# Kernel optimization log

Hardware: AMD Instinct MI355X
Metric: run time of the kernel (lower is better)

The kernel has to match this reference:

```python
import jax, jax.numpy as jnp
import numpy as np

TOP_K = 32
SCALE_FACTOR = 8.0
NEG_INF = -1e18


def setup_inputs() -> dict:
    key = jax.random.key(0)
    kq, kk, kv = jax.random.split(key, 3)
    B, H, S, D = 2, 16, 2048, 64
    q = jax.random.normal(kq, (B, H, S, D), dtype=jnp.float32)
    k = jax.random.normal(kk, (B, H, S, D), dtype=jnp.float32)
    v = jax.random.normal(kv, (B, H, S, D), dtype=jnp.float32)
    return {"q": q, "k": k, "v": v}


def reference(q, k, v):
    # scores: [B, H, Sq, Sk]
    scores = jnp.einsum("bhqd,bhkd->bhqk", q, k) / SCALE_FACTOR
    # torch code clamps top_k against key.size()[-1] == head dim D (quirk);
    # with TOP_K=32 < D=64 the clamp is inactive.
    top_k = min(TOP_K, k.shape[-1])
    topv, _ = jax.lax.top_k(scores, top_k)            # [B,H,Sq,top_k], sorted desc
    thresh = topv[..., -1:]                            # k-th largest per query row
    mask_k = scores < thresh                           # True -> masked out
    scores = jnp.where(mask_k, NEG_INF, scores)
    attn = jax.nn.softmax(scores, axis=-1)
    context = jnp.einsum("bhqk,bhkd->bhqd", attn, v)
    return context, attn, mask_k
```

## Files before the change

kernel.cpp:

```cpp
#include <hip/hip_runtime.h>
#include <math.h>

namespace {
constexpr int kS = 2048;
constexpr int kD = 64;
constexpr int kBH = 32;
constexpr int kTopK = 32;
constexpr int kBins = 4096;
constexpr int kMaxCand = 256;
constexpr int kKeepCap = 64;
constexpr size_t kCtxElems  = (size_t)kBH * kS * kD;
constexpr size_t kAttnElems = (size_t)kBH * kS * kS;
}

__device__ __forceinline__ unsigned sortable_bits(float x) {
  unsigned u = __float_as_uint(x);
  return u ^ ((u & 0x80000000u) ? 0xFFFFFFFFu : 0x80000000u);
}

__global__ __launch_bounds__(256) void qk_scores(const float* __restrict__ q,
                                                 const float* __restrict__ k,
                                                 float* __restrict__ scores) {
  __shared__ float Qs[64][68];
  __shared__ float KsT[64][68];
  const int bh  = blockIdx.z;
  const int q0  = blockIdx.y * 64;
  const int k0  = blockIdx.x * 64;
  const int tid = threadIdx.x;
  const float* qg = q + ((size_t)bh * kS + q0) * kD;
  const float* kg = k + ((size_t)bh * kS + k0) * kD;

#pragma unroll
  for (int rnd = 0; rnd < 4; ++rnd) {
    int flat = rnd * 1024 + tid * 4;
    int r = flat >> 6;
    int c = flat & 63;
    float4 qv = *(const float4*)(qg + r * kD + c);
    *(float4*)(&Qs[r][c]) = qv;
    float4 kv = *(const float4*)(kg + r * kD + c);
    KsT[c + 0][r] = kv.x;
    KsT[c + 1][r] = kv.y;
    KsT[c + 2][r] = kv.z;
    KsT[c + 3][r] = kv.w;
  }
  __syncthreads();

  const int ty = tid >> 4;
  const int tx = tid & 15;
  float acc[4][4] = {};
#pragma unroll
  for (int kk = 0; kk < 64; kk += 4) {
    float4 a[4], b[4];
#pragma unroll
    for (int i = 0; i < 4; ++i) a[i] = *(const float4*)(&Qs[ty * 4 + i][kk]);
#pragma unroll
    for (int u = 0; u < 4; ++u) b[u] = *(const float4*)(&KsT[kk + u][tx * 4]);
    const float* Af = (const float*)a;
    const float* Bf = (const float*)b;
#pragma unroll
    for (int i = 0; i < 4; ++i)
#pragma unroll
      for (int u = 0; u < 4; ++u)
#pragma unroll
        for (int j = 0; j < 4; ++j)
          acc[i][j] += Af[i * 4 + u] * Bf[u * 4 + j];
  }

#pragma unroll
  for (int i = 0; i < 4; ++i) {
    float4 o = make_float4(acc[i][0] * 0.125f, acc[i][1] * 0.125f,
                           acc[i][2] * 0.125f, acc[i][3] * 0.125f);
    *(float4*)(scores + ((size_t)bh * kS + q0 + ty * 4 + i) * kS + k0 + tx * 4) = o;
  }
}

__global__ __launch_bounds__(256) void topk_softmax(const float* __restrict__ v,
                                                    float* __restrict__ ctx,
                                                    float* __restrict__ attn,
                                                    float* __restrict__ mask) {
  const int row  = blockIdx.x;
  const int bh   = row >> 11;
  const int tid  = threadIdx.x;
  const int lane = tid & 63;
  const int wid  = tid >> 6;

  __shared__ unsigned s_hist[kBins];
  __shared__ float    s_cand[kMaxCand];
  __shared__ int      s_kidx[kKeepCap];
  __shared__ float    s_kw[kKeepCap];
  __shared__ float    s_wmax[4], s_wsum[4];
  __shared__ unsigned s_T[4];
  __shared__ unsigned s_nc, s_nk;
  __shared__ int      s_bstar, s_gabove;
  __shared__ float    s_t32;

  const float* srow = attn + (size_t)row * kS;
  float4 l0 = *(const float4*)(srow + tid * 4);
  float4 l1 = *(const float4*)(srow + 1024 + tid * 4);
  float locv[8] = {l0.x, l0.y, l0.z, l0.w, l1.x, l1.y, l1.z, l1.w};
  int   loce[8];
#pragma unroll
  for (int j = 0; j < 8; ++j)
    loce[j] = (j < 4) ? (tid * 4 + j) : (1024 + tid * 4 + (j - 4));
#pragma unroll
  for (int i = 0; i < 4; ++i)
    *(uint4*)(&s_hist[tid * 16 + i * 4]) = make_uint4(0u, 0u, 0u, 0u);
  if (tid == 0) { s_nc = 0u; s_nk = 0u; }
  __syncthreads();

  unsigned bins[8];
  float pmax = locv[0];
#pragma unroll
  for (int j = 0; j < 8; ++j) {
    bins[j] = sortable_bits(locv[j]) >> 20;
    atomicAdd(&s_hist[bins[j]], 1u);
    pmax = fmaxf(pmax, locv[j]);
  }
#pragma unroll
  for (int off = 32; off >= 1; off >>= 1)
    pmax = fmaxf(pmax, __shfl_xor(pmax, off));
  if (lane == 0) s_wmax[wid] = pmax;
  __syncthreads();

  unsigned lsum = 0;
#pragma unroll
  for (int j = 0; j < 16; ++j) lsum += s_hist[tid * 16 + j];
  unsigned sfx = lsum;
#pragma unroll
  for (int off = 1; off < 64; off <<= 1) {
    unsigned z = __shfl_down(sfx, off);
    if (lane + off < 64) sfx += z;
  }
  if (lane == 0) s_T[wid] = sfx;
  __syncthreads();

  unsigned hi = 0;
#pragma unroll
  for (int w = 0; w < 4; ++w)
    if (w > wid) hi += s_T[w];
  unsigned gsfx  = sfx + hi;
  unsigned above = gsfx - lsum;
  if (gsfx >= (unsigned)kTopK && above < (unsigned)kTopK) {
    unsigned run = above;
    for (int j = 15; j >= 0; --j) {
      unsigned h = s_hist[tid * 16 + j];
      if (run < (unsigned)kTopK && run + h >= (unsigned)kTopK) {
        s_bstar  = tid * 16 + j;
        s_gabove = (int)run;
      }
      run += h;
    }
  }
  __syncthreads();
  const int   bstar  = s_bstar;
  const int   gabove = s_gabove;
  const float mx = fmaxf(fmaxf(s_wmax[0], s_wmax[1]),
                         fmaxf(s_wmax[2], s_wmax[3]));

#pragma unroll
  for (int j = 0; j < 8; ++j) {
    if ((int)bins[j] == bstar) {
      unsigned pos = atomicAdd(&s_nc, 1u);
      if (pos < (unsigned)kMaxCand) s_cand[pos] = locv[j];
    }
  }
  __syncthreads();
  const int m2 = (int)min(s_nc, (unsigned)kMaxCand);

  for (int c = tid; c < m2; c += 256) {
    float x = s_cand[c];
    int g = 0, e = 0;
    for (int j2 = 0; j2 < m2; ++j2) {
      float y = s_cand[j2];
      g += (y > x);
      e += (y == x);
    }
    int G = gabove + g;
    if (G < kTopK && G + e >= kTopK) s_t32 = x;
  }
  __syncthreads();
  const float t32 = s_t32;

  float w8[8];
  float psum = 0.0f;
#pragma unroll
  for (int j = 0; j < 8; ++j) {
    bool keep = (locv[j] >= t32);
    float wv = keep ? __expf(locv[j] - mx) : 0.0f;
    w8[j] = wv;
    psum += wv;
    if (keep) {
      unsigned p = atomicAdd(&s_nk, 1u);
      if (p < (unsigned)kKeepCap) { s_kidx[p] = loce[j]; s_kw[p] = wv; }
    }
  }
#pragma unroll
  for (int off = 32; off >= 1; off >>= 1)
    psum += __shfl_xor(psum, off);
  if (lane == 0) s_wsum[wid] = psum;
  __syncthreads();

  const float Z = s_wsum[0] + s_wsum[1] + s_wsum[2] + s_wsum[3];
  const float invZ = 1.0f / Z;

  float* arow = attn + (size_t)row * kS;
  float* mrow = mask + (size_t)row * kS;
  float4 a0 = make_float4(w8[0] * invZ, w8[1] * invZ, w8[2] * invZ, w8[3] * invZ);
  float4 a1 = make_float4(w8[4] * invZ, w8[5] * invZ, w8[6] * invZ, w8[7] * invZ);
  float4 m0 = make_float4(locv[0] >= t32 ? 0.f : 1.f, locv[1] >= t32 ? 0.f : 1.f,
                          locv[2] >= t32 ? 0.f : 1.f, locv[3] >= t32 ? 0.f : 1.f);
  float4 m1 = make_float4(locv[4] >= t32 ? 0.f : 1.f, locv[5] >= t32 ? 0.f : 1.f,
                          locv[6] >= t32 ? 0.f : 1.f, locv[7] >= t32 ? 0.f : 1.f);
  *(float4*)(arow + tid * 4)        = a0;
  *(float4*)(arow + 1024 + tid * 4) = a1;
  *(float4*)(mrow + tid * 4)        = m0;
  *(float4*)(mrow + 1024 + tid * 4) = m1;

  if (tid < kD) {
    const int nk = (int)min(s_nk, (unsigned)kKeepCap);
    float acc = 0.0f;
    for (int c = 0; c < nk; ++c)
      acc += s_kw[c] * v[((size_t)bh * kS + s_kidx[c]) * kD + tid];
    ctx[(size_t)row * kD + tid] = acc * invZ;
  }
}

extern "C" void kernel_launch(void* const* d_in, const int* in_sizes, int n_in,
                              void* d_out, int out_size, void* d_ws, size_t ws_size,
                              hipStream_t stream) {
  const float* q = (const float*)d_in[0];
  const float* k = (const float*)d_in[1];
  const float* v = (const float*)d_in[2];
  float* out  = (float*)d_out;
  float* ctx  = out;
  float* attn = out + kCtxElems;
  float* mask = attn + kAttnElems;

  dim3 g1(kS / 64, kS / 64, kBH);
  qk_scores<<<g1, 256, 0, stream>>>(q, k, attn);
  topk_softmax<<<dim3(kBH * kS), 256, 0, stream>>>(v, ctx, attn, mask);
}
```

Measured before the change: 1.443 ms.

## Keep Q tile resident and stream K tiles with register prefetch

The QK score kernel now gives each block one 64-query tile for a whole head and loops over all 2048 keys in 128-wide tiles. Q is transposed into shared memory once, and the next K tile is prefetched into registers while the current one is computed. Each thread now computes an 8x4 output patch instead of 4x4. This cuts redundant Q loads and raises arithmetic intensity, but the grid shrinks to 1024 blocks that each do much more work, and the loads use more registers.

```diff
diff --git a/kernel.cpp b/kernel.cpp
--- a/kernel.cpp
+++ b/kernel.cpp
@@ -21,56 +21,78 @@
 __global__ __launch_bounds__(256) void qk_scores(const float* __restrict__ q,
                                                  const float* __restrict__ k,
                                                  float* __restrict__ scores) {
-  __shared__ float Qs[64][68];
-  __shared__ float KsT[64][68];
-  const int bh  = blockIdx.z;
-  const int q0  = blockIdx.y * 64;
-  const int k0  = blockIdx.x * 64;
+  __shared__ float QsT[64][72];
+  __shared__ float KsT[64][132];
+  const int bh  = blockIdx.y;
+  const int q0  = blockIdx.x * 64;
   const int tid = threadIdx.x;
   const float* qg = q + ((size_t)bh * kS + q0) * kD;
-  const float* kg = k + ((size_t)bh * kS + k0) * kD;
-
-#pragma unroll
-  for (int rnd = 0; rnd < 4; ++rnd) {
-    int flat = rnd * 1024 + tid * 4;
-    int r = flat >> 6;
-    int c = flat & 63;
-    float4 qv = *(const float4*)(qg + r * kD + c);
-    *(float4*)(&Qs[r][c]) = qv;
-    float4 kv = *(const float4*)(kg + r * kD + c);
-    KsT[c + 0][r] = kv.x;
-    KsT[c + 1][r] = kv.y;
-    KsT[c + 2][r] = kv.z;
-    KsT[c + 3][r] = kv.w;
-  }
-  __syncthreads();
-
-  const int ty = tid >> 4;
-  const int tx = tid & 15;
-  float acc[4][4] = {};
-#pragma unroll
-  for (int kk = 0; kk < 64; kk += 4) {
-    float4 a[4], b[4];
-#pragma unroll
-    for (int i = 0; i < 4; ++i) a[i] = *(const float4*)(&Qs[ty * 4 + i][kk]);
-#pragma unroll
-    for (int u = 0; u < 4; ++u) b[u] = *(const float4*)(&KsT[kk + u][tx * 4]);
-    const float* Af = (const float*)a;
-    const float* Bf = (const float*)b;
-#pragma unroll
-    for (int i = 0; i < 4; ++i)
-#pragma unroll
-      for (int u = 0; u < 4; ++u)
-#pragma unroll
-        for (int j = 0; j < 4; ++j)
-          acc[i][j] += Af[i * 4 + u] * Bf[u * 4 + j];
-  }
-
-#pragma unroll
-  for (int i = 0; i < 4; ++i) {
-    float4 o = make_float4(acc[i][0] * 0.125f, acc[i][1] * 0.125f,
-                           acc[i][2] * 0.125f, acc[i][3] * 0.125f);
-    *(float4*)(scores + ((size_t)bh * kS + q0 + ty * 4 + i) * kS + k0 + tx * 4) = o;
+  const float* kg = k + (size_t)bh * kS * kD;
+
+#pragma unroll
+  for (int p = 0; p < 4; ++p) {
+    int flat = p * 1024 + tid * 4;
+    int r = flat >> 6, c = flat & 63;
+    float4 v4 = *(const float4*)(qg + flat);
+    QsT[c + 0][r] = v4.x;
+    QsT[c + 1][r] = v4.y;
+    QsT[c + 2][r] = v4.z;
+    QsT[c + 3][r] = v4.w;
+  }
+
+  float4 pf[8];
+#pragma unroll
+  for (int p = 0; p < 8; ++p)
+    pf[p] = *(const float4*)(kg + p * 1024 + tid * 4);
+
+  const int ty8 = (tid >> 5) * 8;
+  const int tx4 = (tid & 31) * 4;
+
+  for (int t = 0; t < 16; ++t) {
+    __syncthreads();
+#pragma unroll
+    for (int p = 0; p < 8; ++p) {
+      int flat = p * 1024 + tid * 4;
+      int r = flat >> 6, c = flat & 63;
+      KsT[c + 0][r] = pf[p].x;
+      KsT[c + 1][r] = pf[p].y;
+      KsT[c + 2][r] = pf[p].z;
+      KsT[c + 3][r] = pf[p].w;
+    }
+    __syncthreads();
+    if (t < 15) {
+      const float* kt = kg + (size_t)(t + 1) * 128 * kD;
+#pragma unroll
+      for (int p = 0; p < 8; ++p)
+        pf[p] = *(const float4*)(kt + p * 1024 + tid * 4);
+    }
+
+    float acc[8][4] = {};
+#pragma unroll
+    for (int d4 = 0; d4 < 64; d4 += 4) {
+      float a[4][8], b[4][4];
+#pragma unroll
+      for (int u = 0; u < 4; ++u) {
+        *(float4*)(&a[u][0]) = *(const float4*)(&QsT[d4 + u][ty8]);
+        *(float4*)(&a[u][4]) = *(const float4*)(&QsT[d4 + u][ty8 + 4]);
+        *(float4*)(&b[u][0]) = *(const float4*)(&KsT[d4 + u][tx4]);
+      }
+#pragma unroll
+      for (int i = 0; i < 8; ++i)
+#pragma unroll
+        for (int u = 0; u < 4; ++u)
+#pragma unroll
+          for (int j = 0; j < 4; ++j)
+            acc[i][j] += a[u][i] * b[u][j];
+    }
+
+    const int c0 = t * 128 + tx4;
+#pragma unroll
+    for (int i = 0; i < 8; ++i) {
+      float4 o = make_float4(acc[i][0] * 0.125f, acc[i][1] * 0.125f,
+                             acc[i][2] * 0.125f, acc[i][3] * 0.125f);
+      *(float4*)(scores + ((size_t)bh * kS + q0 + ty8 + i) * kS + c0) = o;
+    }
   }
 }
 
@@ -236,7 +258,7 @@
   float* attn = out + kCtxElems;
   float* mask = attn + kAttnElems;
 
-  dim3 g1(kS / 64, kS / 64, kBH);
+  dim3 g1(kS / 64, kBH);
   qk_scores<<<g1, 256, 0, stream>>>(q, k, attn);
   topk_softmax<<<dim3(kBH * kS), 256, 0, stream>>>(v, ctx, attn, mask);
 }
```

Result: no change. 1.465 ms (+1.5%).
